# Kernel tuning notes

Hardware: AMD Instinct MI355X
Metric: run time of the kernel (lower is better)

The kernel has to match this reference:

```python
import jax, jax.numpy as jnp
import numpy as np

P_ORDER = 3  # cubic B-spline (spline_order in the torch module)


def _make_knots(degree, lo, hi, order):
    # mirrors Transformation.__init__ knot construction
    d = (hi - lo) / (degree - 1)
    return np.linspace(lo - order * d, hi + order * d, degree + 2 * order).astype(np.float32)


def setup_inputs() -> dict:
    key = jax.random.key(0)
    N, V, degree = 500000, 8, 40
    M = degree + P_ORDER - 1  # 42 coefficients per variable
    k1, k2 = jax.random.split(key)
    # data inside the spline range [-3, 3]
    x = jax.random.uniform(k1, (N, V), minval=-2.9, maxval=2.9, dtype=jnp.float32)
    # unrestricted params in the style of compute_starting_values (inverse softplus of increments)
    base = np.linspace(-3.0, 3.0, M).astype(np.float32)
    raw = base.copy()
    raw[1:] = np.log(np.exp(base[1:] - base[:-1]) - 1.0)
    raw_params = jnp.asarray(np.tile(raw[:, None], (1, V)))
    raw_params = raw_params + 0.01 * jax.random.normal(k2, raw_params.shape, dtype=jnp.float32)
    knots = jnp.asarray(np.stack([_make_knots(degree, -3.0, 3.0, P_ORDER) for _ in range(V)], axis=1))  # [46, V]
    return {"x": x, "raw_params": raw_params, "knots": knots}


def _deboor(x, t, c, p):
    # vectorized deBoor evaluation: x [N], knots t [K], coeffs c [K-p-1]
    K = t.shape[0]
    k = jnp.clip(jnp.searchsorted(t, x, side='right') - 1, p, K - p - 2)  # knot span per point
    j = jnp.arange(p + 1)
    d = c[k[:, None] - p + j]  # [N, p+1] local coefficients (gather)
    for r in range(1, p + 1):
        for jj in range(p, r - 1, -1):
            tl = t[jj + k - p]
            tr = t[jj + 1 + k - r]
            alpha = (x - tl) / (tr - tl)
            d = d.at[:, jj].set((1.0 - alpha) * d[:, jj - 1] + alpha * d[:, jj])
    return d[:, p]


def _eval_var(xv, tv, cv):
    p = P_ORDER
    M = cv.shape[0]
    y = _deboor(xv, tv, cv, p)
    # derivative spline: degree p-1, coeffs from first differences of c
    q = p * (cv[1:] - cv[:-1]) / (tv[p + 1:p + M] - tv[1:M])
    dy = _deboor(xv, tv[1:-1], q, p - 1)
    return y, dy


def reference(x, raw_params, knots):
    # restrict_parameters with monotonically_increasing: softplus increments + cumsum
    incr = jnp.concatenate([raw_params[:1], jax.nn.softplus(raw_params[1:])], axis=0)
    c = jnp.cumsum(incr, axis=0)  # [M, V] monotone coefficients
    y, dy = jax.vmap(_eval_var, in_axes=(1, 1, 1), out_axes=1)(x, knots, c)
    log_d = jnp.log(dy)  # log-determinant contribution of the monotone transform
    return y, log_d
```

## Files before the change

### kernel.cpp

```cpp
#include <hip/hip_runtime.h>
#include <cmath>

#define NV    8
#define NM    42
#define NK    46
#define TOT_C (NM * NV)
#define LDS_STRIDE 48

typedef float f32x4 __attribute__((ext_vector_type(4)));

__global__ void prep_kernel(const float* __restrict__ raw,
                            const float* __restrict__ knots,
                            float* __restrict__ c,
                            float* __restrict__ q) {
    __shared__ float s[TOT_C];
    int tid = threadIdx.x;
    if (tid < TOT_C) {
        float r = raw[tid];
        float inc;
        if (tid < NV) {
            inc = r;
        } else {
            inc = (r > 0.f) ? (r + log1pf(expf(-r))) : log1pf(expf(r));
        }
        s[tid] = inc;
    }
    __syncthreads();
    for (int off = 1; off < NM; off <<= 1) {
        float val = 0.f;
        if (tid < TOT_C) {
            int j = tid >> 3;
            val = s[tid] + ((j >= off) ? s[tid - off * NV] : 0.f);
        }
        __syncthreads();
        if (tid < TOT_C) s[tid] = val;
        __syncthreads();
    }
    if (tid < TOT_C) {
        int j = tid >> 3, v = tid & 7;
        float cj = s[tid];
        c[tid] = cj;
        float qj = 0.f;
        if (j < NM - 1) {
            float cn = s[tid + NV];
            qj = 3.f * (cn - cj) / (knots[(j + 4) * NV + v] - knots[(j + 1) * NV + v]);
        }
        q[tid] = qj;
    }
}

__device__ __forceinline__ void eval_one(float xv, int v,
                                         const float* __restrict__ sc,
                                         const float* __restrict__ sq,
                                         const float* __restrict__ st0,
                                         const float* __restrict__ sinvd,
                                         float& yv, float& ldv) {
    float f = (xv - st0[v]) * sinvd[v];
    int k = (int)floorf(f);
    k = min(max(k, 3), NK - 5);
    float u = f - (float)k;
    int base = v * LDS_STRIDE + (k - 3);
    float c0 = sc[base], c1 = sc[base + 1], c2 = sc[base + 2], c3 = sc[base + 3];
    float q0 = sq[base], q1 = sq[base + 1], q2 = sq[base + 2];

    float omu = 1.f - u;
    float u2 = u * u,  o2 = omu * omu;
    float u3 = u2 * u, o3 = o2 * omu;
    const float k6 = 0.16666666666f;
    float B0 = o3 * k6;
    float B3 = u3 * k6;
    float B1 = (3.f * u3 - 6.f * u2 + 4.f) * k6;
    float B2 = 1.f - B0 - B1 - B3;
    yv = fmaf(B0, c0, fmaf(B1, c1, fmaf(B2, c2, B3 * c3)));

    float w0 = 0.5f * o2, w2 = 0.5f * u2, w1 = 1.f - w0 - w2;
    ldv = __logf(fmaf(w0, q0, fmaf(w1, q1, w2 * q2)));
}

__global__ __launch_bounds__(256) void eval_kernel(
        const float* __restrict__ x,
        const float* __restrict__ knots,
        const float* __restrict__ c,
        const float* __restrict__ q,
        float* __restrict__ y_out,
        float* __restrict__ ld_out,
        int total) {
    __shared__ float sc[NV * LDS_STRIDE];
    __shared__ float sq[NV * LDS_STRIDE];
    __shared__ float st0[NV];
    __shared__ float sinvd[NV];
    int tid = threadIdx.x;
    for (int idx = tid; idx < TOT_C; idx += 256) {
        int j = idx >> 3, v = idx & 7;
        sc[v * LDS_STRIDE + j] = c[idx];
        sq[v * LDS_STRIDE + j] = q[idx];
    }
    if (tid < NV) {
        float t0 = knots[tid];
        st0[tid] = t0;
        sinvd[tid] = 1.0f / (knots[NV + tid] - t0);
    }
    __syncthreads();

    int t = blockIdx.x * 256 + tid;
    int i0 = t * 4;
    if (i0 + 3 < total) {
        f32x4 xv = *(const f32x4*)(x + i0);
        int v0 = i0 & (NV - 1);
        float y0, y1, y2, y3, l0, l1, l2, l3;
        eval_one(xv.x, v0,     sc, sq, st0, sinvd, y0, l0);
        eval_one(xv.y, v0 + 1, sc, sq, st0, sinvd, y1, l1);
        eval_one(xv.z, v0 + 2, sc, sq, st0, sinvd, y2, l2);
        eval_one(xv.w, v0 + 3, sc, sq, st0, sinvd, y3, l3);
        f32x4 yv = {y0, y1, y2, y3};
        f32x4 lv = {l0, l1, l2, l3};
        __builtin_nontemporal_store(yv, (f32x4*)(y_out + i0));
        __builtin_nontemporal_store(lv, (f32x4*)(ld_out + i0));
    } else {
        for (int i = i0; i < total; ++i) {
            float yv, lv;
            eval_one(x[i], i & (NV - 1), sc, sq, st0, sinvd, yv, lv);
            y_out[i]  = yv;
            ld_out[i] = lv;
        }
    }
}

extern "C" void kernel_launch(void* const* d_in, const int* in_sizes, int n_in,
                              void* d_out, int out_size, void* d_ws, size_t ws_size,
                              hipStream_t stream) {
    const float* x     = (const float*)d_in[0];
    const float* raw   = (const float*)d_in[1];
    const float* knots = (const float*)d_in[2];

    float* c = (float*)d_ws;
    float* q = c + TOT_C;

    int total = in_sizes[0];
    float* y_out  = (float*)d_out;
    float* ld_out = y_out + total;

    prep_kernel<<<1, 384, 0, stream>>>(raw, knots, c, q);
    int nthreads = (total + 3) / 4;
    int blocks = (nthreads + 255) / 256;
    eval_kernel<<<blocks, 256, 0, stream>>>(x, knots, c, q, y_out, ld_out, total);
}
```

Measured before the change: 82.00 us.

## Fuse coefficient prep into eval kernel, recomputing softplus scan per block

Removes the separate single-block prep kernel and instead has every eval block compute the softplus increments, the prefix sum and the derivative coefficients directly in shared memory. This drops one kernel launch and the serialized dependency between the two kernels. In exchange, every block does redundant transcendental math, roughly six barrier-separated scan steps and the divisions before it can start evaluating points, which lengthens each block's prologue across about 3900 blocks.

```diff
diff --git a/kernel.cpp b/kernel.cpp
--- a/kernel.cpp
+++ b/kernel.cpp
@@ -8,46 +8,6 @@
 #define LDS_STRIDE 48
 
 typedef float f32x4 __attribute__((ext_vector_type(4)));
-
-__global__ void prep_kernel(const float* __restrict__ raw,
-                            const float* __restrict__ knots,
-                            float* __restrict__ c,
-                            float* __restrict__ q) {
-    __shared__ float s[TOT_C];
-    int tid = threadIdx.x;
-    if (tid < TOT_C) {
-        float r = raw[tid];
-        float inc;
-        if (tid < NV) {
-            inc = r;
-        } else {
-            inc = (r > 0.f) ? (r + log1pf(expf(-r))) : log1pf(expf(r));
-        }
-        s[tid] = inc;
-    }
-    __syncthreads();
-    for (int off = 1; off < NM; off <<= 1) {
-        float val = 0.f;
-        if (tid < TOT_C) {
-            int j = tid >> 3;
-            val = s[tid] + ((j >= off) ? s[tid - off * NV] : 0.f);
-        }
-        __syncthreads();
-        if (tid < TOT_C) s[tid] = val;
-        __syncthreads();
-    }
-    if (tid < TOT_C) {
-        int j = tid >> 3, v = tid & 7;
-        float cj = s[tid];
-        c[tid] = cj;
-        float qj = 0.f;
-        if (j < NM - 1) {
-            float cn = s[tid + NV];
-            qj = 3.f * (cn - cj) / (knots[(j + 4) * NV + v] - knots[(j + 1) * NV + v]);
-        }
-        q[tid] = qj;
-    }
-}
 
 __device__ __forceinline__ void eval_one(float xv, int v,
                                          const float* __restrict__ sc,
@@ -77,11 +37,10 @@
     ldv = __logf(fmaf(w0, q0, fmaf(w1, q1, w2 * q2)));
 }
 
-__global__ __launch_bounds__(256) void eval_kernel(
+__global__ __launch_bounds__(256) void fused_kernel(
         const float* __restrict__ x,
+        const float* __restrict__ raw,
         const float* __restrict__ knots,
-        const float* __restrict__ c,
-        const float* __restrict__ q,
         float* __restrict__ y_out,
         float* __restrict__ ld_out,
         int total) {
@@ -90,15 +49,53 @@
     __shared__ float st0[NV];
     __shared__ float sinvd[NV];
     int tid = threadIdx.x;
+
     for (int idx = tid; idx < TOT_C; idx += 256) {
         int j = idx >> 3, v = idx & 7;
-        sc[v * LDS_STRIDE + j] = c[idx];
-        sq[v * LDS_STRIDE + j] = q[idx];
+        float r = raw[idx];
+        float inc;
+        if (j == 0) {
+            inc = r;
+        } else {
+            inc = (r > 0.f) ? (r + log1pf(expf(-r))) : log1pf(expf(r));
+        }
+        sc[v * LDS_STRIDE + j] = inc;
     }
     if (tid < NV) {
         float t0 = knots[tid];
         st0[tid] = t0;
         sinvd[tid] = 1.0f / (knots[NV + tid] - t0);
+    }
+    __syncthreads();
+
+    for (int off = 1; off < NM; off <<= 1) {
+        float val0 = 0.f, val1 = 0.f;
+        int idx0 = tid, idx1 = tid + 256;
+        if (idx0 < TOT_C) {
+            int j = idx0 >> 3, v = idx0 & 7;
+            float s = sc[v * LDS_STRIDE + j];
+            val0 = s + ((j >= off) ? sc[v * LDS_STRIDE + j - off] : 0.f);
+        }
+        if (idx1 < TOT_C) {
+            int j = idx1 >> 3, v = idx1 & 7;
+            float s = sc[v * LDS_STRIDE + j];
+            val1 = s + ((j >= off) ? sc[v * LDS_STRIDE + j - off] : 0.f);
+        }
+        __syncthreads();
+        if (idx0 < TOT_C) { int j = idx0 >> 3, v = idx0 & 7; sc[v * LDS_STRIDE + j] = val0; }
+        if (idx1 < TOT_C) { int j = idx1 >> 3, v = idx1 & 7; sc[v * LDS_STRIDE + j] = val1; }
+        __syncthreads();
+    }
+
+    for (int idx = tid; idx < TOT_C; idx += 256) {
+        int j = idx >> 3, v = idx & 7;
+        float qj = 0.f;
+        if (j < NM - 1) {
+            float cj = sc[v * LDS_STRIDE + j];
+            float cn = sc[v * LDS_STRIDE + j + 1];
+            qj = 3.f * (cn - cj) / (knots[(j + 4) * NV + v] - knots[(j + 1) * NV + v]);
+        }
+        sq[v * LDS_STRIDE + j] = qj;
     }
     __syncthreads();
 
@@ -133,15 +130,11 @@
     const float* raw   = (const float*)d_in[1];
     const float* knots = (const float*)d_in[2];
 
-    float* c = (float*)d_ws;
-    float* q = c + TOT_C;
-
     int total = in_sizes[0];
     float* y_out  = (float*)d_out;
     float* ld_out = y_out + total;
 
-    prep_kernel<<<1, 384, 0, stream>>>(raw, knots, c, q);
     int nthreads = (total + 3) / 4;
     int blocks = (nthreads + 255) / 256;
-    eval_kernel<<<blocks, 256, 0, stream>>>(x, knots, c, q, y_out, ld_out, total);
+    fused_kernel<<<blocks, 256, 0, stream>>>(x, raw, knots, y_out, ld_out, total);
 }
```

Result: slower. 85.29 us (+4.0%).

## Derive derivative from spline coefficients and process eight points per thread

Applied to the files above, without the earlier changes.

Drops the separate derivative-coefficient table q. The derivative is computed on the fly from differences of the four loaded c coefficients, scaled by the uniform inverse knot spacing. Each thread now handles a full row of 8 variables, so variable indices become compile-time template constants, and it uses nontemporal loads. This cuts LDS traffic and staging work, but assumes uniform knot spacing in the derivative formula.

```diff
diff --git a/kernel.cpp b/kernel.cpp
--- a/kernel.cpp
+++ b/kernel.cpp
@@ -10,9 +10,7 @@
 typedef float f32x4 __attribute__((ext_vector_type(4)));
 
 __global__ void prep_kernel(const float* __restrict__ raw,
-                            const float* __restrict__ knots,
-                            float* __restrict__ c,
-                            float* __restrict__ q) {
+                            float* __restrict__ c) {
     __shared__ float s[TOT_C];
     int tid = threadIdx.x;
     if (tid < TOT_C) {
@@ -36,32 +34,22 @@
         if (tid < TOT_C) s[tid] = val;
         __syncthreads();
     }
-    if (tid < TOT_C) {
-        int j = tid >> 3, v = tid & 7;
-        float cj = s[tid];
-        c[tid] = cj;
-        float qj = 0.f;
-        if (j < NM - 1) {
-            float cn = s[tid + NV];
-            qj = 3.f * (cn - cj) / (knots[(j + 4) * NV + v] - knots[(j + 1) * NV + v]);
-        }
-        q[tid] = qj;
-    }
+    if (tid < TOT_C) c[tid] = s[tid];
 }
 
-__device__ __forceinline__ void eval_one(float xv, int v,
+template <int V>
+__device__ __forceinline__ void eval_one(float xv,
                                          const float* __restrict__ sc,
-                                         const float* __restrict__ sq,
                                          const float* __restrict__ st0,
                                          const float* __restrict__ sinvd,
                                          float& yv, float& ldv) {
-    float f = (xv - st0[v]) * sinvd[v];
+    float invd = sinvd[V];
+    float f = (xv - st0[V]) * invd;
     int k = (int)floorf(f);
     k = min(max(k, 3), NK - 5);
     float u = f - (float)k;
-    int base = v * LDS_STRIDE + (k - 3);
+    int base = V * LDS_STRIDE + (k - 3);
     float c0 = sc[base], c1 = sc[base + 1], c2 = sc[base + 2], c3 = sc[base + 3];
-    float q0 = sq[base], q1 = sq[base + 1], q2 = sq[base + 2];
 
     float omu = 1.f - u;
     float u2 = u * u,  o2 = omu * omu;
@@ -74,26 +62,24 @@
     yv = fmaf(B0, c0, fmaf(B1, c1, fmaf(B2, c2, B3 * c3)));
 
     float w0 = 0.5f * o2, w2 = 0.5f * u2, w1 = 1.f - w0 - w2;
-    ldv = __logf(fmaf(w0, q0, fmaf(w1, q1, w2 * q2)));
+    float dy = fmaf(w0, c1 - c0, fmaf(w1, c2 - c1, w2 * (c3 - c2))) * invd;
+    ldv = __logf(dy);
 }
 
 __global__ __launch_bounds__(256) void eval_kernel(
         const float* __restrict__ x,
         const float* __restrict__ knots,
         const float* __restrict__ c,
-        const float* __restrict__ q,
         float* __restrict__ y_out,
         float* __restrict__ ld_out,
         int total) {
     __shared__ float sc[NV * LDS_STRIDE];
-    __shared__ float sq[NV * LDS_STRIDE];
     __shared__ float st0[NV];
     __shared__ float sinvd[NV];
     int tid = threadIdx.x;
     for (int idx = tid; idx < TOT_C; idx += 256) {
         int j = idx >> 3, v = idx & 7;
         sc[v * LDS_STRIDE + j] = c[idx];
-        sq[v * LDS_STRIDE + j] = q[idx];
     }
     if (tid < NV) {
         float t0 = knots[tid];
@@ -103,25 +89,45 @@
     __syncthreads();
 
     int t = blockIdx.x * 256 + tid;
-    int i0 = t * 4;
-    if (i0 + 3 < total) {
-        f32x4 xv = *(const f32x4*)(x + i0);
-        int v0 = i0 & (NV - 1);
-        float y0, y1, y2, y3, l0, l1, l2, l3;
-        eval_one(xv.x, v0,     sc, sq, st0, sinvd, y0, l0);
-        eval_one(xv.y, v0 + 1, sc, sq, st0, sinvd, y1, l1);
-        eval_one(xv.z, v0 + 2, sc, sq, st0, sinvd, y2, l2);
-        eval_one(xv.w, v0 + 3, sc, sq, st0, sinvd, y3, l3);
-        f32x4 yv = {y0, y1, y2, y3};
-        f32x4 lv = {l0, l1, l2, l3};
-        __builtin_nontemporal_store(yv, (f32x4*)(y_out + i0));
-        __builtin_nontemporal_store(lv, (f32x4*)(ld_out + i0));
+    int i0 = t * 8;
+    if (i0 + 7 < total) {
+        f32x4 xa = __builtin_nontemporal_load((const f32x4*)(x + i0));
+        f32x4 xb = __builtin_nontemporal_load((const f32x4*)(x + i0 + 4));
+        float y0,y1,y2,y3,y4,y5,y6,y7, l0,l1,l2,l3,l4,l5,l6,l7;
+        eval_one<0>(xa.x, sc, st0, sinvd, y0, l0);
+        eval_one<1>(xa.y, sc, st0, sinvd, y1, l1);
+        eval_one<2>(xa.z, sc, st0, sinvd, y2, l2);
+        eval_one<3>(xa.w, sc, st0, sinvd, y3, l3);
+        eval_one<4>(xb.x, sc, st0, sinvd, y4, l4);
+        eval_one<5>(xb.y, sc, st0, sinvd, y5, l5);
+        eval_one<6>(xb.z, sc, st0, sinvd, y6, l6);
+        eval_one<7>(xb.w, sc, st0, sinvd, y7, l7);
+        f32x4 ya = {y0, y1, y2, y3}, yb = {y4, y5, y6, y7};
+        f32x4 la = {l0, l1, l2, l3}, lb = {l4, l5, l6, l7};
+        __builtin_nontemporal_store(ya, (f32x4*)(y_out + i0));
+        __builtin_nontemporal_store(yb, (f32x4*)(y_out + i0 + 4));
+        __builtin_nontemporal_store(la, (f32x4*)(ld_out + i0));
+        __builtin_nontemporal_store(lb, (f32x4*)(ld_out + i0 + 4));
     } else {
         for (int i = i0; i < total; ++i) {
-            float yv, lv;
-            eval_one(x[i], i & (NV - 1), sc, sq, st0, sinvd, yv, lv);
-            y_out[i]  = yv;
-            ld_out[i] = lv;
+            int v = i & 7;
+            float invd = sinvd[v];
+            float f = (x[i] - st0[v]) * invd;
+            int k = (int)floorf(f);
+            k = min(max(k, 3), NK - 5);
+            float u = f - (float)k;
+            int base = v * LDS_STRIDE + (k - 3);
+            float c0 = sc[base], c1 = sc[base + 1], c2 = sc[base + 2], c3 = sc[base + 3];
+            float omu = 1.f - u;
+            float u2 = u * u,  o2 = omu * omu;
+            float u3 = u2 * u, o3 = o2 * omu;
+            const float k6 = 0.16666666666f;
+            float B0 = o3 * k6, B3 = u3 * k6;
+            float B1 = (3.f * u3 - 6.f * u2 + 4.f) * k6;
+            float B2 = 1.f - B0 - B1 - B3;
+            y_out[i] = fmaf(B0, c0, fmaf(B1, c1, fmaf(B2, c2, B3 * c3)));
+            float w0 = 0.5f * o2, w2 = 0.5f * u2, w1 = 1.f - w0 - w2;
+            ld_out[i] = __logf(fmaf(w0, c1 - c0, fmaf(w1, c2 - c1, w2 * (c3 - c2))) * invd);
         }
     }
 }
@@ -134,14 +140,13 @@
     const float* knots = (const float*)d_in[2];
 
     float* c = (float*)d_ws;
-    float* q = c + TOT_C;
 
     int total = in_sizes[0];
     float* y_out  = (float*)d_out;
     float* ld_out = y_out + total;
 
-    prep_kernel<<<1, 384, 0, stream>>>(raw, knots, c, q);
-    int nthreads = (total + 3) / 4;
+    prep_kernel<<<1, 384, 0, stream>>>(raw, c);
+    int nthreads = (total + 7) / 8;
     int blocks = (nthreads + 255) / 256;
-    eval_kernel<<<blocks, 256, 0, stream>>>(x, knots, c, q, y_out, ld_out, total);
+    eval_kernel<<<blocks, 256, 0, stream>>>(x, knots, c, y_out, ld_out, total);
 }
```

Result: no change. 82.00 us (-0.0%).
